# Kernel optimization log

Measured on AMD Instinct MI355X. Metric: run time of the kernel, lower is better.

## Reference

```python
import jax, jax.numpy as jnp
import numpy as np

P = 4       # primitives
NF = 36     # non-functor cats (depth <= 1)
NEG = -1e9  # safe -inf
B, N, V, D = 32, 32, 32000, 64


def _build_functor_tables():
    # cat ids: 0..3 primitives; 4..35 depth-1 functors op(res,arg) res,arg<4;
    # remaining: depth-2 functors op(res,arg), res,arg in nf cats, not both primitive.
    def d1(op, res, arg):
        return 4 + op * 16 + res * 4 + arg
    nxt = NF
    d2 = {}
    for op in range(2):
        for res in range(NF):
            for arg in range(NF):
                if res < P and arg < P:
                    continue
                d2[(op, res, arg)] = nxt
                nxt += 1
    C = nxt  # 2596
    def fid(op, res, arg):
        return d1(op, res, arg) if (res < P and arg < P) else d2[(op, res, arg)]
    lf = np.zeros((NF, NF), np.int32)
    rf = np.zeros((NF, NF), np.int32)
    for res in range(NF):
        for arg in range(NF):
            lf[arg, res] = fid(0, res, arg)  # '-b' : functor on the left
            rf[arg, res] = fid(1, res, arg)  # '-a' : functor on the right
    return lf, rf, C


def setup_inputs() -> dict:
    lf, rf, C = _build_functor_tables()
    key = jax.random.key(0)
    ks = jax.random.split(key, 24)
    g = lambda i, shp, s: jax.random.normal(ks[i], shp, dtype=jnp.float32) * s
    inp = {
        "x": jax.random.randint(ks[0], (B, N), 0, V, dtype=jnp.int32),
        "l_functors": jnp.asarray(lf),
        "r_functors": jnp.asarray(rf),
        "root_W": g(1, (1, C), 0.1),
        "root_b": g(2, (C,), 0.1),
        "rule_W": g(3, (NF, 2 * NF), 0.1),
        "rule_b": g(4, (2 * NF,), 0.1),
        "nt_emb": g(5, (C, D), 1.0),
        "sW1": g(6, (D, D), 0.125), "sb1": g(7, (D,), 0.02),
        "r1W1": g(8, (D, D), 0.125), "r1b1": g(9, (D,), 0.02),
        "r1W2": g(10, (D, D), 0.125), "r1b2": g(11, (D,), 0.02),
        "r2W1": g(12, (D, D), 0.125), "r2b1": g(13, (D,), 0.02),
        "r2W2": g(14, (D, D), 0.125), "r2b2": g(15, (D,), 0.02),
        "sW2": g(16, (D, 2), 0.125), "sb2": g(17, (2,), 0.02),
        "vocab_W": g(18, (D, V), 0.125), "vocab_b": g(19, (V,), 0.02),
    }
    return inp


def _res_layer(h, W1, b1, W2, b2):
    return jax.nn.relu(jax.nn.relu(h @ W1 + b1) @ W2 + b2) + h


def reference(x, l_functors, r_functors, root_W, root_b, rule_W, rule_b, nt_emb,
              sW1, sb1, r1W1, r1b1, r1W2, r1b2, r2W1, r2b1, r2W2, r2b2,
              sW2, sb2, vocab_W, vocab_b):
    C = nt_emb.shape[0]
    # --- grammar parameters ---
    root_mask = jnp.where(jnp.arange(C) < P, 0.0, NEG)
    root_scores = jax.nn.log_softmax(root_mask + (root_W[0] + root_b))      # [C]
    rule_scores = jax.nn.log_softmax(rule_W + rule_b, axis=1)               # [NF,2NF] (rule_mlp(eye))
    h = nt_emb @ sW1 + sb1
    h = _res_layer(h, r1W1, r1b1, r1W2, r1b2)
    h = _res_layer(h, r2W1, r2b1, r2W2, r2b2)
    split = jax.nn.log_softmax(h @ sW2 + sb2, axis=1)                       # [C,2]
    G_larg = rule_scores[:, :NF] + split[:NF, 0:1]                          # [res,arg]
    G_rarg = rule_scores[:, NF:] + split[:NF, 0:1]
    # --- emission (word model): log_softmax over vocab, gather word ids ---
    dist = jax.nn.log_softmax(nt_emb @ vocab_W + vocab_b, axis=1)           # [C,V]
    emis = dist[:, x]                                                       # [C,B,N]
    beta1 = jnp.transpose(emis, (2, 1, 0)) + split[:, 1]                    # [N,B,C] lexical inside
    # --- CKY inside algorithm ---
    n = beta1.shape[0]
    lf_c = jnp.minimum(l_functors, NF - 1); l_valid = l_functors < NF
    rf_c = jnp.minimum(r_functors, NF - 1); r_valid = r_functors < NF
    rf1 = beta1[:, :, r_functors]   # [N,B,arg,res] functor score at length-1 spans
    lf1 = beta1[:, :, l_functors]
    Gl = G_larg.T                   # [arg,res]
    Gr = G_rarg.T
    chart = {1: beta1[:, :, :NF]}   # chart[L][i] = inside of span [i, i+L) over nf cats
    for L in range(2, n + 1):
        S = n - L + 1
        terms = []
        for k in range(1, L):  # left length k, right length L-k
            left = chart[k][:S]              # [S,B,NF]
            right = chart[L - k][k:k + S]    # [S,B,NF]
            # case larg: res -> arg (left, nf) + r_functor (right)
            if L - k == 1:
                rF = rf1[k:k + S]
            else:
                rF = jnp.where(r_valid, right[..., rf_c], NEG)
            tA = left[..., :, None] + rF + Gl                       # [S,B,arg,res]
            # case rarg: res -> l_functor (left) + arg (right, nf)
            if k == 1:
                lF = lf1[:S]
            else:
                lF = jnp.where(l_valid, left[..., lf_c], NEG)
            tB = right[..., :, None] + lF + Gr
            terms.append(jax.nn.logsumexp(jnp.concatenate([tA, tB], axis=2), axis=2))
        chart[L] = jax.nn.logsumexp(jnp.stack(terms, 0), axis=0)    # [S,B,NF]
    top = chart[n][0]                                               # [B,NF]
    logprob = jax.nn.logsumexp(top + root_scores[:NF], axis=-1)     # root mask keeps primitives only
    return -logprob
```

## Files before the change

kernel.cpp:

```cpp
#include <hip/hip_runtime.h>
#include <hip/hip_bf16.h>
#include <math.h>

#define CT 2596
#define NF36 36
#define BB 32
#define NN 32
#define VV 32000
#define DD 64
#define NEGF -1e9f
#define NVT 2000

typedef __attribute__((ext_vector_type(8))) short bf16x8;
typedef __attribute__((ext_vector_type(4))) float f32x4;

__device__ __forceinline__ uint32_t f2bf_bits(float x) {
  union { float f; uint32_t u; } v; v.f = x;
  return (v.u + 0x7FFFu + ((v.u >> 16) & 1u)) >> 16;
}
__device__ __forceinline__ float bflo(uint32_t u) {
  union { uint32_t u; float f; } v; v.u = u << 16; return v.f;
}
__device__ __forceinline__ float bfhi(uint32_t u) {
  union { uint32_t u; float f; } v; v.u = u & 0xFFFF0000u; return v.f;
}

__global__ __launch_bounds__(256) void k_front(
    const float* __restrict__ nt_emb,
    const float* __restrict__ sW1, const float* __restrict__ sb1,
    const float* __restrict__ r1W1, const float* __restrict__ r1b1,
    const float* __restrict__ r1W2, const float* __restrict__ r1b2,
    const float* __restrict__ r2W1, const float* __restrict__ r2b1,
    const float* __restrict__ r2W2, const float* __restrict__ r2b2,
    const float* __restrict__ sW2, const float* __restrict__ sb2,
    const float* __restrict__ vocab_W, const float* __restrict__ vocab_b,
    const int* __restrict__ x,
    float* __restrict__ split0, float* __restrict__ split1,
    uint4* __restrict__ Wt, uint4* __restrict__ Bt,
    float* __restrict__ vbt, float* __restrict__ lseacc) {
  int blk = blockIdx.x;
  int tid = threadIdx.x;
  if (blk < 649) {
    __shared__ float hs[4][64], ts[4][64];
    __shared__ float WS[4096];
    int rl = tid >> 6, j = tid & 63;
    int c = blk * 4 + rl;
#define STAGE_W(Wp) for (int q = tid; q < 1024; q += 256) ((float4*)WS)[q] = ((const float4*)(Wp))[q];
    ts[rl][j] = nt_emb[(size_t)c * 64 + j];
    STAGE_W(sW1);
    __syncthreads();
    float a = sb1[j];
#pragma unroll 16
    for (int i = 0; i < 64; i++) a += ts[rl][i] * WS[i * 64 + j];
    __syncthreads();
    hs[rl][j] = a;
    STAGE_W(r1W1);
    __syncthreads();
    float u = r1b1[j];
#pragma unroll 16
    for (int i = 0; i < 64; i++) u += hs[rl][i] * WS[i * 64 + j];
    u = fmaxf(u, 0.f);
    __syncthreads();
    ts[rl][j] = u;
    STAGE_W(r1W2);
    __syncthreads();
    float w = r1b2[j];
#pragma unroll 16
    for (int i = 0; i < 64; i++) w += ts[rl][i] * WS[i * 64 + j];
    w = fmaxf(w, 0.f) + hs[rl][j];
    __syncthreads();
    hs[rl][j] = w;
    STAGE_W(r2W1);
    __syncthreads();
    u = r2b1[j];
#pragma unroll 16
    for (int i = 0; i < 64; i++) u += hs[rl][i] * WS[i * 64 + j];
    u = fmaxf(u, 0.f);
    __syncthreads();
    ts[rl][j] = u;
    STAGE_W(r2W2);
    __syncthreads();
    w = r2b2[j];
#pragma unroll 16
    for (int i = 0; i < 64; i++) w += ts[rl][i] * WS[i * 64 + j];
    w = fmaxf(w, 0.f) + hs[rl][j];
    __syncthreads();
    hs[rl][j] = w;
    __syncthreads();
    if (j < 2) {
      float o = sb2[j];
      for (int i = 0; i < 64; i++) o += hs[rl][i] * sW2[i * 2 + j];
      ts[rl][j] = o;
    }
    __syncthreads();
    if (j < 2) {
      float o0 = ts[rl][0], o1 = ts[rl][1];
      float mx = fmaxf(o0, o1);
      float l = mx + __logf(__expf(o0 - mx) + __expf(o1 - mx));
      if (j == 0) split0[c] = o0 - l;
      else        split1[c] = o1 - l;
    }
#undef STAGE_W
  } else if (blk < 1649) {
    int g = (blk - 649) * 256 + tid;
    int l = g & 63, f = (g >> 6) & 1, vt = g >> 7;
    int v = vt * 16 + (l & 15);
    int kb = f * 32 + 8 * (l >> 4);
    uint32_t d[4];
#pragma unroll
    for (int p = 0; p < 4; p++) {
      float a = vocab_W[(size_t)(kb + 2 * p) * VV + v];
      float b = vocab_W[(size_t)(kb + 2 * p + 1) * VV + v];
      d[p] = f2bf_bits(a) | (f2bf_bits(b) << 16);
    }
    uint4 o; o.x = d[0]; o.y = d[1]; o.z = d[2]; o.w = d[3];
    Wt[g] = o;
  } else if (blk < 1681) {
    int g = (blk - 1649) * 256 + tid;
    int l = g & 63, kf = (g >> 6) & 1, t = g >> 7;
    int j = t * 16 + (l & 15);
    int tok = x[j];
    int kb = kf * 32 + 8 * (l >> 4);
    uint32_t d[4];
#pragma unroll
    for (int p = 0; p < 4; p++) {
      float a = vocab_W[(size_t)(kb + 2 * p) * VV + tok];
      float b = vocab_W[(size_t)(kb + 2 * p + 1) * VV + tok];
      d[p] = f2bf_bits(a) | (f2bf_bits(b) << 16);
    }
    uint4 o; o.x = d[0]; o.y = d[1]; o.z = d[2]; o.w = d[3];
    Bt[g] = o;
    if (g < 1024) vbt[g] = vocab_b[x[g]];
  } else {
    for (int i = tid; i < CT; i += 256) lseacc[i] = 0.f;
  }
}

__global__ __launch_bounds__(128) void k_prelim(
    const float* __restrict__ rule_W, const float* __restrict__ rule_b,
    const float* __restrict__ root_W, const float* __restrict__ root_b,
    const float* __restrict__ split0,
    float* __restrict__ Gl, float* __restrict__ Gr, float* __restrict__ root36) {
  int tid = threadIdx.x;
  int blk = blockIdx.x;
  if (blk < 36) {
    int res = blk;
    __shared__ float red[4];
    float v = (tid < 72) ? rule_W[res * 72 + tid] + rule_b[tid] : -1e30f;
    float m = v;
#pragma unroll
    for (int w = 32; w > 0; w >>= 1) m = fmaxf(m, __shfl_xor(m, w));
    if ((tid & 63) == 0) red[tid >> 6] = m;
    __syncthreads();
    m = fmaxf(red[0], red[1]);
    float e = (tid < 72) ? __expf(v - m) : 0.f;
#pragma unroll
    for (int w = 32; w > 0; w >>= 1) e += __shfl_xor(e, w);
    if ((tid & 63) == 0) red[2 + (tid >> 6)] = e;
    __syncthreads();
    float l = m + __logf(red[2] + red[3]);
    if (tid < 36) {
      float s0 = split0[res];
      Gl[tid * 36 + res] = rule_W[res * 72 + tid] + rule_b[tid] - l + s0;
      Gr[tid * 36 + res] = rule_W[res * 72 + 36 + tid] + rule_b[36 + tid] - l + s0;
    }
  } else {
    __shared__ float lse4s;
    if (tid == 0) {
      float mx = -1e30f;
      for (int i = 0; i < 4; i++) mx = fmaxf(mx, root_W[i] + root_b[i]);
      float ss = 0.f;
      for (int i = 0; i < 4; i++) ss += __expf(root_W[i] + root_b[i] - mx);
      lse4s = mx + __logf(ss);
    }
    __syncthreads();
    if (tid < 36)
      root36[tid] = ((tid < 4) ? 0.f : NEGF) + root_W[tid] + root_b[tid] - lse4s;
  }
}

__global__ __launch_bounds__(256) void k_lse_mfma(
    const float* __restrict__ nt_emb, const uint4* __restrict__ Wt,
    const float* __restrict__ vocab_b, float* __restrict__ lseacc) {
  int tid = threadIdx.x;
  int w = tid >> 6, l = tid & 63;
  int c0 = blockIdx.y * 128;
  int lrow = l & 15, lgrp = l >> 4;

  bf16x8 A[8][2];
#pragma unroll
  for (int ct = 0; ct < 8; ct++) {
    int row = c0 + ct * 16 + lrow;
#pragma unroll
    for (int kf = 0; kf < 2; kf++) {
      bf16x8 fr;
      if (row < CT) {
        const float4* src = (const float4*)(nt_emb + (size_t)row * 64 + kf * 32 + lgrp * 8);
        float4 s0 = src[0], s1 = src[1];
        fr[0] = (short)f2bf_bits(s0.x); fr[1] = (short)f2bf_bits(s0.y);
        fr[2] = (short)f2bf_bits(s0.z); fr[3] = (short)f2bf_bits(s0.w);
        fr[4] = (short)f2bf_bits(s1.x); fr[5] = (short)f2bf_bits(s1.y);
        fr[6] = (short)f2bf_bits(s1.z); fr[7] = (short)f2bf_bits(s1.w);
      } else {
#pragma unroll
        for (int e = 0; e < 8; e++) fr[e] = 0;
      }
      A[ct][kf] = fr;
    }
  }

  float sums[8][4];
#pragma unroll
  for (int ct = 0; ct < 8; ct++)
#pragma unroll
    for (int i = 0; i < 4; i++) sums[ct][i] = 0.f;

  int t0 = blockIdx.x * 80;
  for (int t = t0 + w; t < t0 + 80; t += 4) {
    union { uint4 u; bf16x8 h; } b0, b1;
    b0.u = Wt[(size_t)(t * 2) * 64 + l];
    b1.u = Wt[(size_t)(t * 2 + 1) * 64 + l];
    float vb = vocab_b[t * 16 + lrow];
#pragma unroll
    for (int ct = 0; ct < 8; ct++) {
      f32x4 acc = {0.f, 0.f, 0.f, 0.f};
      acc = __builtin_amdgcn_mfma_f32_16x16x32_bf16(A[ct][0], b0.h, acc, 0, 0, 0);
      acc = __builtin_amdgcn_mfma_f32_16x16x32_bf16(A[ct][1], b1.h, acc, 0, 0, 0);
#pragma unroll
      for (int i = 0; i < 4; i++) sums[ct][i] += __expf(acc[i] + vb);
    }
  }

#pragma unroll
  for (int ct = 0; ct < 8; ct++)
#pragma unroll
    for (int i = 0; i < 4; i++) {
      float v = sums[ct][i];
      v += __shfl_xor(v, 1);
      v += __shfl_xor(v, 2);
      v += __shfl_xor(v, 4);
      v += __shfl_xor(v, 8);
      sums[ct][i] = v;
    }
  if (lrow == 0) {
#pragma unroll
    for (int ct = 0; ct < 8; ct++)
#pragma unroll
      for (int i = 0; i < 4; i++) {
        int row = c0 + ct * 16 + lgrp * 4 + i;
        if (row < CT) atomicAdd(&lseacc[row], sums[ct][i]);
      }
  }
}

__global__ __launch_bounds__(256) void k_beta1_mfma(
    const float* __restrict__ nt_emb, const uint4* __restrict__ Bt,
    const float* __restrict__ vbt, const float* __restrict__ lseacc,
    const float* __restrict__ split1, float* __restrict__ beta1) {
  int tid = threadIdx.x;
  int w = tid >> 6, l = tid & 63;
  int c0 = blockIdx.x * 64;
  int lrow = l & 15, lgrp = l >> 4;
  __shared__ float addS[64];
  if (tid < 64) {
    int row = c0 + tid;
    addS[tid] = (row < CT) ? (split1[row] - __logf(lseacc[row])) : 0.f;
  }

  bf16x8 A[4][2];
#pragma unroll
  for (int ct = 0; ct < 4; ct++) {
    int row = c0 + ct * 16 + lrow;
#pragma unroll
    for (int kf = 0; kf < 2; kf++) {
      bf16x8 fr;
      if (row < CT) {
        const float4* src = (const float4*)(nt_emb + (size_t)row * 64 + kf * 32 + lgrp * 8);
        float4 s0 = src[0], s1 = src[1];
        fr[0] = (short)f2bf_bits(s0.x); fr[1] = (short)f2bf_bits(s0.y);
        fr[2] = (short)f2bf_bits(s0.z); fr[3] = (short)f2bf_bits(s0.w);
        fr[4] = (short)f2bf_bits(s1.x); fr[5] = (short)f2bf_bits(s1.y);
        fr[6] = (short)f2bf_bits(s1.z); fr[7] = (short)f2bf_bits(s1.w);
      } else {
#pragma unroll
        for (int e = 0; e < 8; e++) fr[e] = 0;
      }
      A[ct][kf] = fr;
    }
  }
  __syncthreads();
  float addv[4][4];
#pragma unroll
  for (int ct = 0; ct < 4; ct++)
#pragma unroll
    for (int i = 0; i < 4; i++) addv[ct][i] = addS[ct * 16 + lgrp * 4 + i];

  int t0 = blockIdx.y * 8;
  for (int t = t0 + w; t < t0 + 8; t += 4) {
    union { uint4 u; bf16x8 h; } b0, b1;
    b0.u = Bt[t * 128 + l];
    b1.u = Bt[t * 128 + 64 + l];
    int j = t * 16 + lrow;
    float vb = vbt[j];
    int jc = (j & 31) * 32 + (j >> 5);
    float* outb = beta1 + (size_t)jc * CT;
#pragma unroll
    for (int ct = 0; ct < 4; ct++) {
      f32x4 acc = {0.f, 0.f, 0.f, 0.f};
      acc = __builtin_amdgcn_mfma_f32_16x16x32_bf16(A[ct][0], b0.h, acc, 0, 0, 0);
      acc = __builtin_amdgcn_mfma_f32_16x16x32_bf16(A[ct][1], b1.h, acc, 0, 0, 0);
      int r0 = c0 + ct * 16 + lgrp * 4;
      if (r0 + 3 < CT) {
        float4 o;
        o.x = acc[0] + vb + addv[ct][0];
        o.y = acc[1] + vb + addv[ct][1];
        o.z = acc[2] + vb + addv[ct][2];
        o.w = acc[3] + vb + addv[ct][3];
        *(float4*)(outb + r0) = o;
      } else {
        for (int i = 0; i < 4; i++)
          if (r0 + i < CT) outb[r0 + i] = acc[i] + vb + addv[ct][i];
      }
    }
  }
}

__global__ __launch_bounds__(256) void k_edge(
    const float* __restrict__ beta1, const int* __restrict__ lf_t,
    const int* __restrict__ rf_t, const float* __restrict__ Gl,
    const float* __restrict__ Gr,
    uint32_t* __restrict__ elB, uint32_t* __restrict__ erB) {
  int sb = blockIdx.x;
  const float* brow = beta1 + (size_t)sb * CT;
  size_t ob = (size_t)sb * 720;
  for (int wd = threadIdx.x; wd < 720; wd += 256) {
    int res = wd / 20, p = wd - res * 20;
    int a0 = 2 * p, a1 = 2 * p + 1;
    uint32_t l0 = 0, l1 = 0, r0 = 0, r1 = 0;
    if (a0 < 36) {
      int i0 = a0 * 36 + res;
      l0 = f2bf_bits(__expf(brow[lf_t[i0]] + Gr[i0]));
      r0 = f2bf_bits(__expf(brow[rf_t[i0]] + Gl[i0]));
    }
    if (a1 < 36) {
      int i1 = a1 * 36 + res;
      l1 = f2bf_bits(__expf(brow[lf_t[i1]] + Gr[i1]));
      r1 = f2bf_bits(__expf(brow[rf_t[i1]] + Gl[i1]));
    }
    elB[ob + wd] = l0 | (l1 << 16);
    erB[ob + wd] = r0 | (r1 << 16);
  }
}

__global__ __launch_bounds__(1024, 4) void k_cky(
    const float* __restrict__ beta1, const uint32_t* __restrict__ elB,
    const uint32_t* __restrict__ erB, const float* __restrict__ Gl,
    const float* __restrict__ Gr, const float* __restrict__ root36,
    float* __restrict__ out) {
  __shared__ __align__(16) float D[19008];
  __shared__ float Mt[528];
  __shared__ __align__(16) float PA[1280], PB[1280];
  __shared__ __align__(16) float Ec1lT[512], Ec1rT[512];
  __shared__ __align__(16) float eGlT[16], eGrT[16];
  __shared__ unsigned int candb[2][33];
  __shared__ float MIDacc[128];

  int b = blockIdx.x, tid = threadIdx.x;

  if (tid < 66) candb[tid / 33][tid % 33] = 0u;
  if (tid < 32) Mt[tid] = 0.f;
  if (tid < 16) {
    int res = tid >> 2, a = tid & 3;
    eGlT[tid] = __expf(Gl[a * 36 + res]);
    eGrT[tid] = __expf(Gr[a * 36 + res]);
  }
  for (int i = tid; i < 1280; i += 1024) { PA[i] = 0.f; PB[i] = 0.f; }
  __syncthreads();
  for (int i = tid; i < 32 * 36; i += 1024) {
    int s = i / 36;
    float v = __expf(beta1[(size_t)(s * 32 + b) * CT + (i - s * 36)]);
    D[i] = v;
    atomicMax(&candb[1][s], __float_as_uint(v));
  }
  __syncthreads();
  for (int i = tid; i < 512; i += 1024) {
    int s = i >> 4, rr = (i >> 2) & 3, a = i & 3;
    float d1 = D[s * 36 + a];
    Ec1lT[i] = d1 * eGlT[rr * 4 + a];
    Ec1rT[i] = d1 * eGrT[rr * 4 + a];
  }
  __syncthreads();

  for (int L = 2; L <= 32; L++) {
    int S = 33 - L;
    int offL  = 36 * (((L - 1) * (66 - L)) >> 1);
    int offP  = 36 * (((L - 2) * (67 - L)) >> 1);
    int offML = ((L - 1) * (66 - L)) >> 1;
    int offMP = ((L - 2) * (67 - L)) >> 1;
    int par = L & 1, parP = par ^ 1;

    if (tid < 33) candb[par][tid] = 0u;
    if (tid >= 64 && tid < 192) MIDacc[tid - 64] = 0.f;
    int totA = S * 36;
    for (int o = tid; o < totA; o += 1024) {
      int s = o / 36, j = o - s * 36;
      float MtA = Mt[offMP + s], MtB = Mt[offMP + s + 1];
      float cA = MtA + __logf(fmaxf(__uint_as_float(candb[parP][s]), 1e-37f));
      float cB = MtB + __logf(fmaxf(__uint_as_float(candb[parP][s + 1]), 1e-37f));
      float Mn = fmaxf(cA, cB);
      PA[s * 40 + j] = D[offP + s * 36 + j] * __expf(MtA - Mn);
      PB[s * 40 + j] = D[offP + (s + 1) * 36 + j] * __expf(MtB - Mn);
      if (j == 0) Mt[offML + s] = Mn;
    }
    __syncthreads();

    int tot = S * 36;
    int nmid = (L >= 4) ? 4 * S * (L - 3) : 0;
    int W = tot + nmid;
    for (int o = tid; o < W; o += 1024) {
      if (o < tot) {
        int s = o / 36, res = o - s * 36;
        const uint4* el4 = (const uint4*)(elB + (size_t)(s * 32 + b) * 720 + res * 20);
        const uint4* er4 = (const uint4*)(erB + (size_t)((s + L - 1) * 32 + b) * 720 + res * 20);
        const float4* pB4 = (const float4*)(PB + s * 40);
        const float4* pA4 = (const float4*)(PA + s * 40);
        float a0 = 0.f, a1 = 0.f, a2 = 0.f, a3 = 0.f;
#pragma unroll
        for (int q = 0; q < 5; q++) {
          uint4 u = el4[q];
          float4 p0 = pB4[2 * q], p1 = pB4[2 * q + 1];
          a0 = fmaf(bflo(u.x), p0.x, a0); a1 = fmaf(bfhi(u.x), p0.y, a1);
          a2 = fmaf(bflo(u.y), p0.z, a2); a3 = fmaf(bfhi(u.y), p0.w, a3);
          a0 = fmaf(bflo(u.z), p1.x, a0); a1 = fmaf(bfhi(u.z), p1.y, a1);
          a2 = fmaf(bflo(u.w), p1.z, a2); a3 = fmaf(bfhi(u.w), p1.w, a3);
          uint4 v = er4[q];
          float4 q0 = pA4[2 * q], q1 = pA4[2 * q + 1];
          a0 = fmaf(bflo(v.x), q0.x, a0); a1 = fmaf(bfhi(v.x), q0.y, a1);
          a2 = fmaf(bflo(v.y), q0.z, a2); a3 = fmaf(bfhi(v.y), q0.w, a3);
          a0 = fmaf(bflo(v.z), q1.x, a0); a1 = fmaf(bfhi(v.z), q1.y, a1);
          a2 = fmaf(bflo(v.w), q1.z, a2); a3 = fmaf(bfhi(v.w), q1.w, a3);
        }
        if (res < 4 && L >= 3) {
          const float4* ecl = (const float4*)(Ec1lT + s * 16 + res * 4);
          const float4* ecr = (const float4*)(Ec1rT + (s + L - 1) * 16 + res * 4);
          float4 e0 = ecl[0], pb = pB4[5 + res];
          float4 e1 = ecr[0], pa = pA4[1 + res];
          a0 = fmaf(e0.x, pb.x, a0); a1 = fmaf(e0.y, pb.y, a1);
          a2 = fmaf(e0.z, pb.z, a2); a3 = fmaf(e0.w, pb.w, a3);
          a0 = fmaf(e1.x, pa.x, a0); a1 = fmaf(e1.y, pa.y, a1);
          a2 = fmaf(e1.z, pa.z, a2); a3 = fmaf(e1.w, pa.w, a3);
        }
        float val = (a0 + a1) + (a2 + a3);
        D[offL + o] = val;
        atomicMax(&candb[par][s], __float_as_uint(val));
      } else {
        int o2 = o - tot;
        int kidx = o2 / (4 * S);
        int rem = o2 - kidx * 4 * S;
        int s = rem >> 2, res = rem & 3;
        int k = kidx + 2;
        int lk = L - k;
        int tk = ((k - 1) * (66 - k)) >> 1;
        int tl = ((lk - 1) * (66 - lk)) >> 1;
        const float4* Dk4 = (const float4*)(D + 36 * tk + s * 36);
        const float4* Dl4 = (const float4*)(D + 36 * tl + (s + k) * 36);
        float4 dk0 = Dk4[0], dkh = Dk4[1 + res];
        float4 dl0 = Dl4[0], dlh = Dl4[5 + res];
        float4 egl = ((const float4*)eGlT)[res];
        float4 egr = ((const float4*)eGrT)[res];
        float f = __expf(Mt[tk + s] + Mt[tl + s + k] - Mt[offML + s]);
        float sub = dk0.x * dlh.x * egl.x + dk0.y * dlh.y * egl.y
                  + dk0.z * dlh.z * egl.z + dk0.w * dlh.w * egl.w
                  + dl0.x * dkh.x * egr.x + dl0.y * dkh.y * egr.y
                  + dl0.z * dkh.z * egr.z + dl0.w * dkh.w * egr.w;
        atomicAdd(&MIDacc[rem], f * sub);
      }
    }
    __syncthreads();

    if (L >= 4) {
      for (int o = tid; o < 4 * S; o += 1024) {
        int s = o >> 2;
        float nv = D[offL + s * 36 + (o & 3)] + MIDacc[o];
        D[offL + s * 36 + (o & 3)] = nv;
        atomicMax(&candb[par][s], __float_as_uint(nv));
      }
    }
    __syncthreads();
  }

  int wid = tid >> 6, lane = tid & 63;
  if (wid == 0) {
    int off32 = 36 * ((31 * 34) >> 1);
    float v = (lane < 36) ? D[off32 + lane] * __expf(root36[lane]) : 0.f;
#pragma unroll
    for (int w = 32; w > 0; w >>= 1) v += __shfl_xor(v, w);
    if (lane == 0) out[b] = -(Mt[527] + __logf(v));
  }
}

extern "C" void kernel_launch(void* const* d_in, const int* in_sizes, int n_in,
                              void* d_out, int out_size, void* d_ws, size_t ws_size,
                              hipStream_t stream) {
  const int*   x       = (const int*)d_in[0];
  const int*   lf_t    = (const int*)d_in[1];
  const int*   rf_t    = (const int*)d_in[2];
  const float* root_W  = (const float*)d_in[3];
  const float* root_b  = (const float*)d_in[4];
  const float* rule_W  = (const float*)d_in[5];
  const float* rule_b  = (const float*)d_in[6];
  const float* nt_emb  = (const float*)d_in[7];
  const float* sW1     = (const float*)d_in[8];
  const float* sb1     = (const float*)d_in[9];
  const float* r1W1    = (const float*)d_in[10];
  const float* r1b1    = (const float*)d_in[11];
  const float* r1W2    = (const float*)d_in[12];
  const float* r1b2    = (const float*)d_in[13];
  const float* r2W1    = (const float*)d_in[14];
  const float* r2b1    = (const float*)d_in[15];
  const float* r2W2    = (const float*)d_in[16];
  const float* r2b2    = (const float*)d_in[17];
  const float* sW2     = (const float*)d_in[18];
  const float* sb2     = (const float*)d_in[19];
  const float* vocab_W = (const float*)d_in[20];
  const float* vocab_b = (const float*)d_in[21];
  float* outp = (float*)d_out;

  float* ws = (float*)d_ws;
  float* split0 = ws;
  float* split1 = ws + 2596;
  float* Gl     = ws + 5192;
  float* Gr     = ws + 6488;
  float* root36 = ws + 7784;
  float* lseacc = ws + 7848;
  float* vbt    = ws + 10448;
  float* beta1  = ws + 11472;
  uint32_t* elB = (uint32_t*)(ws + 2669776);
  uint32_t* erB = (uint32_t*)(ws + 3407056);
  uint4* Wt     = (uint4*)(ws + 2669776);
  uint4* Bt     = (uint4*)(ws + 4144336);

  k_front<<<1682, 256, 0, stream>>>(nt_emb, sW1, sb1, r1W1, r1b1, r1W2, r1b2,
                                    r2W1, r2b1, r2W2, r2b2, sW2, sb2,
                                    vocab_W, vocab_b, x,
                                    split0, split1, Wt, Bt, vbt, lseacc);
  k_prelim<<<37, 128, 0, stream>>>(rule_W, rule_b, root_W, root_b, split0,
                                   Gl, Gr, root36);
  k_lse_mfma<<<dim3(25, 21), 256, 0, stream>>>(nt_emb, Wt, vocab_b, lseacc);
  k_beta1_mfma<<<dim3(41, 8), 256, 0, stream>>>(nt_emb, Bt, vbt, lseacc, split1, beta1);
  k_edge<<<1024, 256, 0, stream>>>(beta1, lf_t, rf_t, Gl, Gr, elB, erB);
  k_cky<<<32, 1024, 0, stream>>>(beta1, elB, erB, Gl, Gr, root36, outp);
}
```

Before: 202.7 us.

## Fold prelim kernel into front kernel, cache left-edge rows in registers

Moves the rule-softmax and root-score computation into extra blocks of the front kernel, removing a separate launch. The split0 term is now added later in the edge and CKY kernels rather than baked into Gl/Gr. The CKY kernel preloads each thread's left-edge bf16 row into registers once instead of reloading it every span length, and splits the MID atomic accumulator into two banks to reduce contention. The trade-off is higher register pressure in the 1024-thread CKY kernel.

```diff
diff --git a/kernel.cpp b/kernel.cpp
--- a/kernel.cpp
+++ b/kernel.cpp
@@ -9,7 +9,6 @@
 #define VV 32000
 #define DD 64
 #define NEGF -1e9f
-#define NVT 2000
 
 typedef __attribute__((ext_vector_type(8))) short bf16x8;
 typedef __attribute__((ext_vector_type(4))) float f32x4;
@@ -35,9 +34,13 @@
     const float* __restrict__ sW2, const float* __restrict__ sb2,
     const float* __restrict__ vocab_W, const float* __restrict__ vocab_b,
     const int* __restrict__ x,
+    const float* __restrict__ rule_W, const float* __restrict__ rule_b,
+    const float* __restrict__ root_W, const float* __restrict__ root_b,
     float* __restrict__ split0, float* __restrict__ split1,
     uint4* __restrict__ Wt, uint4* __restrict__ Bt,
-    float* __restrict__ vbt, float* __restrict__ lseacc) {
+    float* __restrict__ vbt, float* __restrict__ lseacc,
+    float* __restrict__ Gl, float* __restrict__ Gr,
+    float* __restrict__ root36) {
   int blk = blockIdx.x;
   int tid = threadIdx.x;
   if (blk < 649) {
@@ -131,38 +134,27 @@
     uint4 o; o.x = d[0]; o.y = d[1]; o.z = d[2]; o.w = d[3];
     Bt[g] = o;
     if (g < 1024) vbt[g] = vocab_b[x[g]];
-  } else {
+  } else if (blk == 1681) {
     for (int i = tid; i < CT; i += 256) lseacc[i] = 0.f;
-  }
-}
-
-__global__ __launch_bounds__(128) void k_prelim(
-    const float* __restrict__ rule_W, const float* __restrict__ rule_b,
-    const float* __restrict__ root_W, const float* __restrict__ root_b,
-    const float* __restrict__ split0,
-    float* __restrict__ Gl, float* __restrict__ Gr, float* __restrict__ root36) {
-  int tid = threadIdx.x;
-  int blk = blockIdx.x;
-  if (blk < 36) {
-    int res = blk;
-    __shared__ float red[4];
+  } else if (blk < 1718) {
+    int res = blk - 1682;
+    __shared__ float red[8];
     float v = (tid < 72) ? rule_W[res * 72 + tid] + rule_b[tid] : -1e30f;
     float m = v;
 #pragma unroll
     for (int w = 32; w > 0; w >>= 1) m = fmaxf(m, __shfl_xor(m, w));
     if ((tid & 63) == 0) red[tid >> 6] = m;
     __syncthreads();
-    m = fmaxf(red[0], red[1]);
+    m = fmaxf(fmaxf(red[0], red[1]), fmaxf(red[2], red[3]));
     float e = (tid < 72) ? __expf(v - m) : 0.f;
 #pragma unroll
     for (int w = 32; w > 0; w >>= 1) e += __shfl_xor(e, w);
-    if ((tid & 63) == 0) red[2 + (tid >> 6)] = e;
-    __syncthreads();
-    float l = m + __logf(red[2] + red[3]);
+    if ((tid & 63) == 0) red[4 + (tid >> 6)] = e;
+    __syncthreads();
+    float l = m + __logf(red[4] + red[5] + red[6] + red[7]);
     if (tid < 36) {
-      float s0 = split0[res];
-      Gl[tid * 36 + res] = rule_W[res * 72 + tid] + rule_b[tid] - l + s0;
-      Gr[tid * 36 + res] = rule_W[res * 72 + 36 + tid] + rule_b[36 + tid] - l + s0;
+      Gl[tid * 36 + res] = rule_W[res * 72 + tid] + rule_b[tid] - l;
+      Gr[tid * 36 + res] = rule_W[res * 72 + 36 + tid] + rule_b[36 + tid] - l;
     }
   } else {
     __shared__ float lse4s;
@@ -328,24 +320,25 @@
 __global__ __launch_bounds__(256) void k_edge(
     const float* __restrict__ beta1, const int* __restrict__ lf_t,
     const int* __restrict__ rf_t, const float* __restrict__ Gl,
-    const float* __restrict__ Gr,
+    const float* __restrict__ Gr, const float* __restrict__ split0,
     uint32_t* __restrict__ elB, uint32_t* __restrict__ erB) {
   int sb = blockIdx.x;
   const float* brow = beta1 + (size_t)sb * CT;
   size_t ob = (size_t)sb * 720;
   for (int wd = threadIdx.x; wd < 720; wd += 256) {
     int res = wd / 20, p = wd - res * 20;
+    float s0 = split0[res];
     int a0 = 2 * p, a1 = 2 * p + 1;
     uint32_t l0 = 0, l1 = 0, r0 = 0, r1 = 0;
     if (a0 < 36) {
       int i0 = a0 * 36 + res;
-      l0 = f2bf_bits(__expf(brow[lf_t[i0]] + Gr[i0]));
-      r0 = f2bf_bits(__expf(brow[rf_t[i0]] + Gl[i0]));
+      l0 = f2bf_bits(__expf(brow[lf_t[i0]] + Gr[i0] + s0));
+      r0 = f2bf_bits(__expf(brow[rf_t[i0]] + Gl[i0] + s0));
     }
     if (a1 < 36) {
       int i1 = a1 * 36 + res;
-      l1 = f2bf_bits(__expf(brow[lf_t[i1]] + Gr[i1]));
-      r1 = f2bf_bits(__expf(brow[rf_t[i1]] + Gl[i1]));
+      l1 = f2bf_bits(__expf(brow[lf_t[i1]] + Gr[i1] + s0));
+      r1 = f2bf_bits(__expf(brow[rf_t[i1]] + Gl[i1] + s0));
     }
     elB[ob + wd] = l0 | (l1 << 16);
     erB[ob + wd] = r0 | (r1 << 16);
@@ -355,24 +348,33 @@
 __global__ __launch_bounds__(1024, 4) void k_cky(
     const float* __restrict__ beta1, const uint32_t* __restrict__ elB,
     const uint32_t* __restrict__ erB, const float* __restrict__ Gl,
-    const float* __restrict__ Gr, const float* __restrict__ root36,
-    float* __restrict__ out) {
+    const float* __restrict__ Gr, const float* __restrict__ split0,
+    const float* __restrict__ root36, float* __restrict__ out) {
   __shared__ __align__(16) float D[19008];
   __shared__ float Mt[528];
   __shared__ __align__(16) float PA[1280], PB[1280];
   __shared__ __align__(16) float Ec1lT[512], Ec1rT[512];
   __shared__ __align__(16) float eGlT[16], eGrT[16];
   __shared__ unsigned int candb[2][33];
-  __shared__ float MIDacc[128];
+  __shared__ float MIDacc[2][128];
 
   int b = blockIdx.x, tid = threadIdx.x;
+  int tS = tid / 36, tR = tid - tS * 36;
+
+  uint4 elc[5];
+  {
+    const uint4* el4 = (const uint4*)(elB + (size_t)(tS * 32 + b) * 720 + tR * 20);
+#pragma unroll
+    for (int q = 0; q < 5; q++) elc[q] = el4[q];
+  }
 
   if (tid < 66) candb[tid / 33][tid % 33] = 0u;
   if (tid < 32) Mt[tid] = 0.f;
   if (tid < 16) {
     int res = tid >> 2, a = tid & 3;
-    eGlT[tid] = __expf(Gl[a * 36 + res]);
-    eGrT[tid] = __expf(Gr[a * 36 + res]);
+    float s0 = split0[res];
+    eGlT[tid] = __expf(Gl[a * 36 + res] + s0);
+    eGrT[tid] = __expf(Gr[a * 36 + res] + s0);
   }
   for (int i = tid; i < 1280; i += 1024) { PA[i] = 0.f; PB[i] = 0.f; }
   __syncthreads();
@@ -400,7 +402,7 @@
     int par = L & 1, parP = par ^ 1;
 
     if (tid < 33) candb[par][tid] = 0u;
-    if (tid >= 64 && tid < 192) MIDacc[tid - 64] = 0.f;
+    if (tid >= 64 && tid < 320) MIDacc[(tid - 64) >> 7][(tid - 64) & 127] = 0.f;
     int totA = S * 36;
     for (int o = tid; o < totA; o += 1024) {
       int s = o / 36, j = o - s * 36;
@@ -420,14 +422,22 @@
     for (int o = tid; o < W; o += 1024) {
       if (o < tot) {
         int s = o / 36, res = o - s * 36;
-        const uint4* el4 = (const uint4*)(elB + (size_t)(s * 32 + b) * 720 + res * 20);
+        uint4 u5[5];
+        if (o == tid) {
+#pragma unroll
+          for (int q = 0; q < 5; q++) u5[q] = elc[q];
+        } else {
+          const uint4* el4 = (const uint4*)(elB + (size_t)(s * 32 + b) * 720 + res * 20);
+#pragma unroll
+          for (int q = 0; q < 5; q++) u5[q] = el4[q];
+        }
         const uint4* er4 = (const uint4*)(erB + (size_t)((s + L - 1) * 32 + b) * 720 + res * 20);
         const float4* pB4 = (const float4*)(PB + s * 40);
         const float4* pA4 = (const float4*)(PA + s * 40);
         float a0 = 0.f, a1 = 0.f, a2 = 0.f, a3 = 0.f;
 #pragma unroll
         for (int q = 0; q < 5; q++) {
-          uint4 u = el4[q];
+          uint4 u = u5[q];
           float4 p0 = pB4[2 * q], p1 = pB4[2 * q + 1];
           a0 = fmaf(bflo(u.x), p0.x, a0); a1 = fmaf(bfhi(u.x), p0.y, a1);
           a2 = fmaf(bflo(u.y), p0.z, a2); a3 = fmaf(bfhi(u.y), p0.w, a3);
@@ -473,7 +483,7 @@
                   + dk0.z * dlh.z * egl.z + dk0.w * dlh.w * egl.w
                   + dl0.x * dkh.x * egr.x + dl0.y * dkh.y * egr.y
                   + dl0.z * dkh.z * egr.z + dl0.w * dkh.w * egr.w;
-        atomicAdd(&MIDacc[rem], f * sub);
+        atomicAdd(&MIDacc[kidx & 1][rem], f * sub);
       }
     }
     __syncthreads();
@@ -481,7 +491,7 @@
     if (L >= 4) {
       for (int o = tid; o < 4 * S; o += 1024) {
         int s = o >> 2;
-        float nv = D[offL + s * 36 + (o & 3)] + MIDacc[o];
+        float nv = D[offL + s * 36 + (o & 3)] + MIDacc[0][o] + MIDacc[1][o];
         D[offL + s * 36 + (o & 3)] = nv;
         atomicMax(&candb[par][s], __float_as_uint(nv));
       }
@@ -540,14 +550,14 @@
   uint4* Wt     = (uint4*)(ws + 2669776);
   uint4* Bt     = (uint4*)(ws + 4144336);
 
-  k_front<<<1682, 256, 0, stream>>>(nt_emb, sW1, sb1, r1W1, r1b1, r1W2, r1b2,
+  k_front<<<1719, 256, 0, stream>>>(nt_emb, sW1, sb1, r1W1, r1b1, r1W2, r1b2,
                                     r2W1, r2b1, r2W2, r2b2, sW2, sb2,
                                     vocab_W, vocab_b, x,
-                                    split0, split1, Wt, Bt, vbt, lseacc);
-  k_prelim<<<37, 128, 0, stream>>>(rule_W, rule_b, root_W, root_b, split0,
-                                   Gl, Gr, root36);
+                                    rule_W, rule_b, root_W, root_b,
+                                    split0, split1, Wt, Bt, vbt, lseacc,
+                                    Gl, Gr, root36);
   k_lse_mfma<<<dim3(25, 21), 256, 0, stream>>>(nt_emb, Wt, vocab_b, lseacc);
   k_beta1_mfma<<<dim3(41, 8), 256, 0, stream>>>(nt_emb, Bt, vbt, lseacc, split1, beta1);
-  k_edge<<<1024, 256, 0, stream>>>(beta1, lf_t, rf_t, Gl, Gr, elB, erB);
-  k_cky<<<32, 1024, 0, stream>>>(beta1, elB, erB, Gl, Gr, root36, outp);
-}
+  k_edge<<<1024, 256, 0, stream>>>(beta1, lf_t, rf_t, Gl, Gr, split0, elB, erB);
+  k_cky<<<32, 1024, 0, stream>>>(beta1, elB, erB, Gl, Gr, split0, root36, outp);
+}
```

After: 264.3 us. +30.4%, slower.
